# Optimization experiments

Hardware: AMD Instinct MI355X
Metric: run time of the kernel (lower is better)

## Reference

```python
import math
import jax, jax.numpy as jnp
import numpy as np

NUM_HEADS = 16
NEG = -1e30  # block-causal 'invisible' value (stand-in for -inf)
SCALES = [(1, 1, 1), (1, 2, 2), (1, 4, 4), (1, 8, 8), (1, 16, 16), (1, 32, 32)]


def _block_causal_bias(L):
    blocks = np.array([t * h * w for (t, h, w) in SCALES])
    cum = np.cumsum(blocks)  # visible kv length for each scale block
    per_query_visible = np.repeat(cum, blocks)  # (L,)
    cols = np.arange(L)
    mask = np.where(cols[None, :] < per_query_visible[:, None], 0.0, NEG).astype(np.float32)
    return jnp.asarray(mask)[None, None]  # (1,1,L,L)


def _rope_tables(L, half_dim):
    # 2D-rope-style cos/sin tables; exact frequency layout is data, math is the rotation
    pos = np.arange(L, dtype=np.float32)
    inv_freq = 1.0 / (10000.0 ** (np.arange(half_dim, dtype=np.float32) / half_dim))
    ang = pos[:, None] * inv_freq[None, :]  # (L, half_dim)
    return jnp.asarray(np.cos(ang)), jnp.asarray(np.sin(ang))


def setup_inputs() -> dict:
    key = jax.random.key(0)
    ks = jax.random.split(key, 6)
    B, C, H = 4, 1024, NUM_HEADS
    hd = C // H
    L = int(sum(t * h * w for (t, h, w) in SCALES))  # 1365
    x = jax.random.normal(ks[0], (B, L, C), dtype=jnp.float32)
    attn_bias = _block_causal_bias(L)
    rope_cos, rope_sin = _rope_tables(L, hd // 2)
    W_qkv = jax.random.normal(ks[1], (3 * C, C), dtype=jnp.float32) * (C ** -0.5)
    q_bias = jnp.zeros((C,), dtype=jnp.float32)
    v_bias = jnp.zeros((C,), dtype=jnp.float32)
    scale_mul_log = jnp.full((1, H, 1, 1), math.log(4.0), dtype=jnp.float32)
    W_proj = jax.random.normal(ks[2], (C, C), dtype=jnp.float32) * (C ** -0.5)
    b_proj = jnp.zeros((C,), dtype=jnp.float32)
    return {"x": x, "attn_bias": attn_bias, "rope_cos": rope_cos, "rope_sin": rope_sin,
            "W_qkv": W_qkv, "q_bias": q_bias, "v_bias": v_bias,
            "scale_mul_log": scale_mul_log, "W_proj": W_proj, "b_proj": b_proj}


def _apply_rope(t, rope_cos, rope_sin):
    # t: (B,H,L,hd) -> rotate consecutive pairs with per-position cos/sin
    B, H, L, hd = t.shape
    t2 = t.reshape(B, H, L, hd // 2, 2)
    c = rope_cos[None, None]  # (1,1,L,hd/2)
    s = rope_sin[None, None]
    r0 = c * t2[..., 0] - s * t2[..., 1]
    r1 = s * t2[..., 0] + c * t2[..., 1]
    return jnp.stack([r0, r1], axis=-1).reshape(B, H, L, hd)


def reference(x, attn_bias, rope_cos, rope_sin, W_qkv, q_bias, v_bias,
              scale_mul_log, W_proj, b_proj):
    B, L, C = x.shape
    H = NUM_HEADS
    hd = C // H
    # QKV with custom bias construction: (q_bias, zeros, v_bias)
    bias = jnp.concatenate([q_bias, jnp.zeros_like(q_bias), v_bias])
    qkv = (x @ W_qkv.T + bias).reshape(B, L, 3, H, hd)
    qkv = jnp.transpose(qkv, (2, 0, 3, 1, 4))  # (3,B,H,L,hd)
    q, k, v = qkv[0], qkv[1], qkv[2]
    # cos-attn: L2-normalize q,k; q scaled by clamped learnable per-head temperature
    max_scale_mul = math.log(100.0)
    scale_mul = jnp.exp(jnp.minimum(scale_mul_log, max_scale_mul))  # (1,H,1,1)
    q = q / jnp.maximum(jnp.linalg.norm(q, axis=-1, keepdims=True), 1e-12) * scale_mul
    k = k / jnp.maximum(jnp.linalg.norm(k, axis=-1, keepdims=True), 1e-12)
    # inline RoPE on q and k
    q = _apply_rope(q, rope_cos, rope_sin)
    k = _apply_rope(k, rope_cos, rope_sin)
    # block-causal attention; softmax scale = 1 under cos_attn
    logits = jnp.einsum('bhqd,bhkd->bhqk', q, k) + attn_bias
    attn = jax.nn.softmax(logits, axis=-1)
    out = jnp.einsum('bhqk,bhkd->bhqd', attn, v)
    out = jnp.transpose(out, (0, 2, 1, 3)).reshape(B, L, C)
    return out @ W_proj.T + b_proj
```

## Files before the change

### kernel.cpp

```cpp
#include <hip/hip_runtime.h>

typedef __bf16 bf16_t;
typedef __bf16 bf16x8 __attribute__((ext_vector_type(8)));
typedef float f32x4 __attribute__((ext_vector_type(4)));

#define B_SZ 4
#define NHEADS 16
#define L_SEQ 1365
#define LP_V 1408
#define C_DIM 1024
#define HD 64
#define M_ROWS (B_SZ * L_SEQ)
#define K_DIM 1024
#define BHL (B_SZ * NHEADS * L_SEQ)

__device__ __forceinline__ f32x4 zero4() {
    f32x4 z; z[0] = 0.f; z[1] = 0.f; z[2] = 0.f; z[3] = 0.f; return z;
}

__device__ __forceinline__ void gload_lds16(const void* g, void* l) {
    __builtin_amdgcn_global_load_lds(
        (const __attribute__((address_space(1))) void*)(uintptr_t)g,
        (__attribute__((address_space(3))) void*)(unsigned int)(uintptr_t)l,
        16, 0, 0);
}

__device__ __forceinline__ int vislen(int row) {
    if (row < 1) return 1;
    if (row < 5) return 5;
    if (row < 21) return 21;
    if (row < 85) return 85;
    if (row < 341) return 341;
    return 1365;
}

#define N8_X  (5591040 / 8)
#define N8_WQ (3145728 / 8)
#define N8_WP (1048576 / 8)
__global__ __launch_bounds__(256) void cvt_all(const float* __restrict__ x,
                                               const float* __restrict__ wq,
                                               const float* __restrict__ wp,
                                               bf16_t* __restrict__ xo,
                                               bf16_t* __restrict__ wqo,
                                               bf16_t* __restrict__ wpo) {
    int i = blockIdx.x * 256 + threadIdx.x;
    const float* in;
    bf16_t* out;
    if (i < N8_X) { in = x; out = xo; }
    else if (i < N8_X + N8_WQ) { i -= N8_X; in = wq; out = wqo; }
    else if (i < N8_X + N8_WQ + N8_WP) { i -= N8_X + N8_WQ; in = wp; out = wpo; }
    else return;
    const float* p = in + (size_t)i * 8;
    f32x4 a = *(const f32x4*)p;
    f32x4 b = *(const f32x4*)(p + 4);
    bf16x8 r;
    r[0] = (bf16_t)a[0]; r[1] = (bf16_t)a[1]; r[2] = (bf16_t)a[2]; r[3] = (bf16_t)a[3];
    r[4] = (bf16_t)b[0]; r[5] = (bf16_t)b[1]; r[6] = (bf16_t)b[2]; r[7] = (bf16_t)b[3];
    *(bf16x8*)(out + (size_t)i * 8) = r;
}

__global__ __launch_bounds__(256) void qkv_gemm(const bf16_t* __restrict__ A,
                                                const bf16_t* __restrict__ Bw,
                                                const float* __restrict__ qbias,
                                                const float* __restrict__ vbias,
                                                bf16_t* __restrict__ qo,
                                                bf16_t* __restrict__ ko,
                                                bf16_t* __restrict__ vt) {
    __shared__ __align__(16) bf16_t As[128 * 32];
    __shared__ __align__(16) bf16_t Bs[128 * 32];
    const int tid = threadIdx.x;
    const int w = tid >> 6, lane = tid & 63, quad = lane >> 4, l16 = lane & 15;
    const int id = blockIdx.x;
    const int xcd = id & 7, s = id >> 3;
    const int ntile = xcd * 3 + s / 43;
    const int mtile = s - (s / 43) * 43;
    const int mw = (w >> 1) * 64, nw = (w & 1) * 64;

    int ar0 = mtile * 128 + (tid >> 2); if (ar0 > M_ROWS - 1) ar0 = M_ROWS - 1;
    int ar1 = ar0 + 64;                 if (ar1 > M_ROWS - 1) ar1 = M_ROWS - 1;
    const int nr0 = ntile * 128 + (tid >> 2);
    const int cc = (tid & 3) * 8;

    f32x4 acc[4][4];
#pragma unroll
    for (int i = 0; i < 4; ++i)
#pragma unroll
        for (int j = 0; j < 4; ++j) acc[i][j] = zero4();

    for (int k0 = 0; k0 < K_DIM; k0 += 32) {
        __syncthreads();
        gload_lds16(A + (size_t)ar0 * K_DIM + k0 + cc, (char*)As + tid * 16);
        gload_lds16(A + (size_t)ar1 * K_DIM + k0 + cc, (char*)As + tid * 16 + 4096);
        gload_lds16(Bw + (size_t)nr0 * K_DIM + k0 + cc, (char*)Bs + tid * 16);
        gload_lds16(Bw + (size_t)(nr0 + 64) * K_DIM + k0 + cc, (char*)Bs + tid * 16 + 4096);
        __syncthreads();
        bf16x8 af[4], bfr[4];
#pragma unroll
        for (int mi = 0; mi < 4; ++mi)
            af[mi] = *(const bf16x8*)&As[(mw + mi * 16 + l16) * 32 + quad * 8];
#pragma unroll
        for (int ni = 0; ni < 4; ++ni)
            bfr[ni] = *(const bf16x8*)&Bs[(nw + ni * 16 + l16) * 32 + quad * 8];
#pragma unroll
        for (int mi = 0; mi < 4; ++mi)
#pragma unroll
            for (int ni = 0; ni < 4; ++ni)
                acc[mi][ni] = __builtin_amdgcn_mfma_f32_16x16x32_bf16(af[mi], bfr[ni], acc[mi][ni], 0, 0, 0);
    }

#pragma unroll
    for (int ni = 0; ni < 4; ++ni) {
        int ncol = ntile * 128 + nw + ni * 16 + l16;
        int three = ncol >> 10;
        int rem = ncol & 1023;
        int h = rem >> 6, d = rem & 63;
        float bias = 0.f;
        if (three == 0) bias = qbias[rem];
        else if (three == 2) bias = vbias[rem];
        bf16_t* dst = (three == 0) ? qo : ((three == 1) ? ko : vt);
#pragma unroll
        for (int mi = 0; mi < 4; ++mi)
#pragma unroll
            for (int r = 0; r < 4; ++r) {
                int grow = mtile * 128 + mw + mi * 16 + quad * 4 + r;
                if (grow < M_ROWS) {
                    int b_ = grow / L_SEQ;
                    int l = grow - b_ * L_SEQ;
                    dst[(((size_t)(b_ * NHEADS + h)) * L_SEQ + l) * HD + d] =
                        (bf16_t)(acc[mi][ni][r] + bias);
                }
            }
    }
}

__global__ __launch_bounds__(256) void vtrans(const bf16_t* __restrict__ in,
                                              bf16_t* __restrict__ out) {
    __shared__ bf16_t t[64][64];
    const int lt = blockIdx.x * 64, bh = blockIdx.y;
    const int tid = threadIdx.x;
#pragma unroll
    for (int it = 0; it < 2; ++it) {
        const int r = (tid >> 3) + it * 32, c8 = (tid & 7) * 8;
        int l = lt + r; if (l > L_SEQ - 1) l = L_SEQ - 1;
        bf16x8 v8 = *(const bf16x8*)(in + ((size_t)bh * L_SEQ + l) * HD + c8);
#pragma unroll
        for (int j = 0; j < 8; ++j) t[c8 + j][r] = v8[j];
    }
    __syncthreads();
#pragma unroll
    for (int it = 0; it < 2; ++it) {
        int c = tid + it * 256;
        int d = c >> 3, off = (c & 7) * 8;
        bf16x8 o8 = *(const bf16x8*)&t[d][off];
        *(bf16x8*)(out + ((size_t)bh * HD + d) * LP_V + lt + off) = o8;
    }
}

__global__ __launch_bounds__(256) void normrope(bf16_t* __restrict__ qb,
                                                bf16_t* __restrict__ kb,
                                                const float* __restrict__ cosb,
                                                const float* __restrict__ sinb,
                                                const float* __restrict__ sml) {
    const int tid = threadIdx.x;
    const int w = tid >> 6, lane = tid & 63;
    int vi = blockIdx.x * 4 + w;
    bool isq = vi < BHL;
    int idx = isq ? vi : (vi - BHL);
    bf16_t* buf = isq ? qb : kb;
    int bh = idx / L_SEQ;
    int l = idx - bh * L_SEQ;
    int h = bh & (NHEADS - 1);
    size_t base = (size_t)idx * HD;

    float v = (float)buf[base + lane];
    float ss = v * v;
#pragma unroll
    for (int off = 1; off < 64; off <<= 1) ss += __shfl_xor(ss, off);
    float nrm = fmaxf(sqrtf(ss), 1e-12f);
    v = v / nrm;
    if (isq) {
        float s = expf(fminf(sml[h], 4.6051702f));
        v *= s;
    }
    int i = lane >> 1;
    float c = cosb[l * 32 + i];
    float s2 = sinb[l * 32 + i];
    float p = __shfl_xor(v, 1);
    float r = (lane & 1) ? (s2 * p + c * v) : (c * v - s2 * p);
    buf[base + lane] = (bf16_t)r;
}

__global__ __launch_bounds__(256) void attn(const bf16_t* __restrict__ q,
                                            const bf16_t* __restrict__ k,
                                            const bf16_t* __restrict__ v,
                                            bf16_t* __restrict__ ao) {
    __shared__ __align__(16) bf16_t plds[4][2][16][72];
    const int tid = threadIdx.x;
    const int w = tid >> 6, lane = tid & 63, quad = lane >> 4, l16 = lane & 15;
    const int id = blockIdx.x;
    const int xcd = id & 7, s0 = id >> 3;
    const int bh = (xcd << 3) + s0 / 11;
    const int gblk = s0 - (s0 / 11) * 11;
    const int g = gblk + 11 * w;
    if (g >= 43) return;
    const int qbase = g * 32;

    bf16x8 aq[2][2];
#pragma unroll
    for (int h = 0; h < 2; ++h) {
        int mrow = qbase + h * 16 + l16;
        int mc = mrow < L_SEQ ? mrow : (L_SEQ - 1);
        const bf16_t* qp = q + ((size_t)bh * L_SEQ + mc) * HD + quad * 8;
        aq[h][0] = *(const bf16x8*)(qp);
        aq[h][1] = *(const bf16x8*)(qp + 32);
    }

    f32x4 o[2][4];
    float l_i[2][4];
    int visr[2][4];
#pragma unroll
    for (int h = 0; h < 2; ++h)
#pragma unroll
        for (int r = 0; r < 4; ++r) {
            o[h][r] = zero4();
            l_i[h][r] = 0.f;
            visr[h][r] = vislen(qbase + h * 16 + quad * 4 + r);
        }

    int rl = qbase + 31; if (rl > L_SEQ - 1) rl = L_SEQ - 1;
    const int ntk = (vislen(rl) + 63) >> 6;

    for (int kt = 0; kt < ntk; ++kt) {
        const int kvb = kt * 64;
        bf16x8 kf0[4], kf1[4];
#pragma unroll
        for (int nb = 0; nb < 4; ++nb) {
            int n = kvb + nb * 16 + l16;
            int nc = n < L_SEQ ? n : (L_SEQ - 1);
            const bf16_t* kp = k + ((size_t)bh * L_SEQ + nc) * HD + quad * 8;
            kf0[nb] = *(const bf16x8*)(kp);
            kf1[nb] = *(const bf16x8*)(kp + 32);
        }
        f32x4 s[2][4];
#pragma unroll
        for (int h = 0; h < 2; ++h)
#pragma unroll
            for (int nb = 0; nb < 4; ++nb) {
                s[h][nb] = zero4();
                s[h][nb] = __builtin_amdgcn_mfma_f32_16x16x32_bf16(aq[h][0], kf0[nb], s[h][nb], 0, 0, 0);
                s[h][nb] = __builtin_amdgcn_mfma_f32_16x16x32_bf16(aq[h][1], kf1[nb], s[h][nb], 0, 0, 0);
            }

#pragma unroll
        for (int h = 0; h < 2; ++h)
#pragma unroll
            for (int nb = 0; nb < 4; ++nb) {
                int col = kvb + nb * 16 + l16;
#pragma unroll
                for (int r = 0; r < 4; ++r) {
                    float e = __expf(s[h][nb][r]);
                    float p = (col < visr[h][r]) ? e : 0.f;
                    l_i[h][r] += p;
                    plds[w][h][quad * 4 + r][nb * 16 + l16] = (bf16_t)p;
                }
            }
        bf16x8 ap[2][2];
#pragma unroll
        for (int h = 0; h < 2; ++h) {
            ap[h][0] = *(const bf16x8*)&plds[w][h][l16][quad * 8];
            ap[h][1] = *(const bf16x8*)&plds[w][h][l16][32 + quad * 8];
        }
#pragma unroll
        for (int nb = 0; nb < 4; ++nb) {
            const bf16_t* vp = v + ((size_t)bh * HD + nb * 16 + l16) * LP_V + kvb + quad * 8;
            bf16x8 v0 = *(const bf16x8*)(vp);
            bf16x8 v1 = *(const bf16x8*)(vp + 32);
#pragma unroll
            for (int h = 0; h < 2; ++h) {
                o[h][nb] = __builtin_amdgcn_mfma_f32_16x16x32_bf16(ap[h][0], v0, o[h][nb], 0, 0, 0);
                o[h][nb] = __builtin_amdgcn_mfma_f32_16x16x32_bf16(ap[h][1], v1, o[h][nb], 0, 0, 0);
            }
        }
    }

    const int b_ = bh >> 4, hh = bh & 15;
#pragma unroll
    for (int h = 0; h < 2; ++h)
#pragma unroll
        for (int r = 0; r < 4; ++r) {
            float ls = l_i[h][r];
#pragma unroll
            for (int off = 1; off < 16; off <<= 1) ls += __shfl_xor(ls, off);
            int rowq = qbase + h * 16 + quad * 4 + r;
            if (rowq < L_SEQ) {
                float inv = 1.f / ls;
#pragma unroll
                for (int nb = 0; nb < 4; ++nb) {
                    int d = nb * 16 + l16;
                    size_t di = ((size_t)(b_ * L_SEQ + rowq)) * C_DIM + hh * HD + d;
                    ao[di] = (bf16_t)(o[h][nb][r] * inv);
                }
            }
        }
}

__global__ __launch_bounds__(256) void proj_gemm(const bf16_t* __restrict__ A,
                                                 const bf16_t* __restrict__ Bw,
                                                 const float* __restrict__ bias,
                                                 float* __restrict__ out) {
    __shared__ __align__(16) bf16_t As[128 * 32];
    __shared__ __align__(16) bf16_t Bs[128 * 32];
    const int tid = threadIdx.x;
    const int w = tid >> 6, lane = tid & 63, quad = lane >> 4, l16 = lane & 15;
    const int id = blockIdx.x;
    const int ntile = id & 7, mtile = id >> 3;
    const int mw = (w >> 1) * 64, nw = (w & 1) * 64;

    int ar0 = mtile * 128 + (tid >> 2); if (ar0 > M_ROWS - 1) ar0 = M_ROWS - 1;
    int ar1 = ar0 + 64;                 if (ar1 > M_ROWS - 1) ar1 = M_ROWS - 1;
    const int nr0 = ntile * 128 + (tid >> 2);
    const int cc = (tid & 3) * 8;

    f32x4 acc[4][4];
#pragma unroll
    for (int i = 0; i < 4; ++i)
#pragma unroll
        for (int j = 0; j < 4; ++j) acc[i][j] = zero4();

    for (int k0 = 0; k0 < K_DIM; k0 += 32) {
        __syncthreads();
        gload_lds16(A + (size_t)ar0 * K_DIM + k0 + cc, (char*)As + tid * 16);
        gload_lds16(A + (size_t)ar1 * K_DIM + k0 + cc, (char*)As + tid * 16 + 4096);
        gload_lds16(Bw + (size_t)nr0 * K_DIM + k0 + cc, (char*)Bs + tid * 16);
        gload_lds16(Bw + (size_t)(nr0 + 64) * K_DIM + k0 + cc, (char*)Bs + tid * 16 + 4096);
        __syncthreads();
        bf16x8 af[4], bfr[4];
#pragma unroll
        for (int mi = 0; mi < 4; ++mi)
            af[mi] = *(const bf16x8*)&As[(mw + mi * 16 + l16) * 32 + quad * 8];
#pragma unroll
        for (int ni = 0; ni < 4; ++ni)
            bfr[ni] = *(const bf16x8*)&Bs[(nw + ni * 16 + l16) * 32 + quad * 8];
#pragma unroll
        for (int mi = 0; mi < 4; ++mi)
#pragma unroll
            for (int ni = 0; ni < 4; ++ni)
                acc[mi][ni] = __builtin_amdgcn_mfma_f32_16x16x32_bf16(af[mi], bfr[ni], acc[mi][ni], 0, 0, 0);
    }

#pragma unroll
    for (int ni = 0; ni < 4; ++ni) {
        int ncol = ntile * 128 + nw + ni * 16 + l16;
        float bv = bias[ncol];
#pragma unroll
        for (int mi = 0; mi < 4; ++mi)
#pragma unroll
            for (int r = 0; r < 4; ++r) {
                int grow = mtile * 128 + mw + mi * 16 + quad * 4 + r;
                if (grow < M_ROWS)
                    out[(size_t)grow * C_DIM + ncol] = acc[mi][ni][r] + bv;
            }
    }
}

extern "C" void kernel_launch(void* const* d_in, const int* in_sizes, int n_in,
                              void* d_out, int out_size, void* d_ws, size_t ws_size,
                              hipStream_t stream) {
    const float* x    = (const float*)d_in[0];
    const float* rc   = (const float*)d_in[2];
    const float* rs   = (const float*)d_in[3];
    const float* Wqkv = (const float*)d_in[4];
    const float* qb   = (const float*)d_in[5];
    const float* vb   = (const float*)d_in[6];
    const float* sml  = (const float*)d_in[7];
    const float* Wp   = (const float*)d_in[8];
    const float* bp   = (const float*)d_in[9];
    float* out = (float*)d_out;

    const size_t NQ   = (size_t)B_SZ * NHEADS * L_SEQ * HD;
    const size_t NVT  = (size_t)B_SZ * NHEADS * HD * LP_V;
    const size_t NX   = (size_t)M_ROWS * C_DIM;
    const size_t NWQ  = (size_t)3 * C_DIM * C_DIM;
    const size_t NWP  = (size_t)C_DIM * C_DIM;

    bf16_t* qo   = (bf16_t*)d_ws;
    bf16_t* ko   = qo + NQ;
    bf16_t* vtmp = ko + NQ;
    bf16_t* vo   = vtmp + NQ;
    bf16_t* xb   = vo + NVT;
    bf16_t* ao   = xb;
    bf16_t* wqb  = xb + NX;
    bf16_t* wpb  = wqb + NWQ;

    dim3 blk(256);
    const int ncvt = (N8_X + N8_WQ + N8_WP + 255) / 256;
    cvt_all<<<dim3(ncvt), blk, 0, stream>>>(x, Wqkv, Wp, xb, wqb, wpb);
    qkv_gemm<<<dim3(1032), blk, 0, stream>>>(xb, wqb, qb, vb, qo, ko, vtmp);
    normrope<<<dim3((2 * BHL) / 4), blk, 0, stream>>>(qo, ko, rc, rs, sml);
    vtrans<<<dim3(22, 64), blk, 0, stream>>>(vtmp, vo);
    attn<<<dim3(704), blk, 0, stream>>>(qo, ko, vo, ao);
    proj_gemm<<<dim3(344), blk, 0, stream>>>(ao, wpb, bp, out);
}
```

Baseline: 335.9 us.

## Fuse norm+RoPE into QKV epilogue and split-KV the last attention scale

Removes the separate normrope kernel by applying L2 norm, per-head temperature and RoPE in the QKV GEMM epilogue using cross-lane shuffles. Attention work is rebalanced: the long last-scale query groups (vislen 1365) are split into two KV chunks written as fp32 partials and combined by a new attn_reduce kernel, while short groups write output directly. This targets load imbalance in attention and the extra q/k round trip through memory, at the cost of partial-buffer traffic and an extra launch. Split partials are summed without max rescaling, which relies on the bounded cos-attn logits.

```diff
diff --git a/kernel.cpp b/kernel.cpp
--- a/kernel.cpp
+++ b/kernel.cpp
@@ -13,6 +13,11 @@
 #define M_ROWS (B_SZ * L_SEQ)
 #define K_DIM 1024
 #define BHL (B_SZ * NHEADS * L_SEQ)
+
+#define NSPLIT 33
+#define NCHUNK 2
+#define UPB (10 + NSPLIT * NCHUNK)
+#define NBLK_ATTN (64 * UPB / 4)
 
 __device__ __forceinline__ f32x4 zero4() {
     f32x4 z; z[0] = 0.f; z[1] = 0.f; z[2] = 0.f; z[3] = 0.f; return z;
@@ -63,6 +68,9 @@
                                                 const bf16_t* __restrict__ Bw,
                                                 const float* __restrict__ qbias,
                                                 const float* __restrict__ vbias,
+                                                const float* __restrict__ rc,
+                                                const float* __restrict__ rs,
+                                                const float* __restrict__ sml,
                                                 bf16_t* __restrict__ qo,
                                                 bf16_t* __restrict__ ko,
                                                 bf16_t* __restrict__ vt) {
@@ -108,26 +116,63 @@
                 acc[mi][ni] = __builtin_amdgcn_mfma_f32_16x16x32_bf16(af[mi], bfr[ni], acc[mi][ni], 0, 0, 0);
     }
 
-#pragma unroll
-    for (int ni = 0; ni < 4; ++ni) {
-        int ncol = ntile * 128 + nw + ni * 16 + l16;
-        int three = ncol >> 10;
-        int rem = ncol & 1023;
-        int h = rem >> 6, d = rem & 63;
-        float bias = 0.f;
-        if (three == 0) bias = qbias[rem];
-        else if (three == 2) bias = vbias[rem];
-        bf16_t* dst = (three == 0) ? qo : ((three == 1) ? ko : vt);
+    const int three = ntile >> 3;
+    const int h = (((ntile & 7) * 128 + nw) >> 6);
+
+    if (three == 2) {
+#pragma unroll
+        for (int ni = 0; ni < 4; ++ni) {
+            int d = ni * 16 + l16;
+            float bv = vbias[h * 64 + d];
+#pragma unroll
+            for (int mi = 0; mi < 4; ++mi)
+#pragma unroll
+                for (int r = 0; r < 4; ++r) {
+                    int grow = mtile * 128 + mw + mi * 16 + quad * 4 + r;
+                    if (grow < M_ROWS) {
+                        int b_ = grow / L_SEQ;
+                        int l = grow - b_ * L_SEQ;
+                        vt[(((size_t)(b_ * NHEADS + h)) * L_SEQ + l) * HD + d] =
+                            (bf16_t)(acc[mi][ni][r] + bv);
+                    }
+                }
+        }
+    } else {
+        float scale = 1.f;
+        if (three == 0) scale = __expf(fminf(sml[h], 4.6051702f));
+        float bias[4];
+#pragma unroll
+        for (int ni = 0; ni < 4; ++ni)
+            bias[ni] = (three == 0) ? qbias[h * 64 + ni * 16 + l16] : 0.f;
+        bf16_t* dst = (three == 0) ? qo : ko;
 #pragma unroll
         for (int mi = 0; mi < 4; ++mi)
 #pragma unroll
             for (int r = 0; r < 4; ++r) {
                 int grow = mtile * 128 + mw + mi * 16 + quad * 4 + r;
-                if (grow < M_ROWS) {
-                    int b_ = grow / L_SEQ;
-                    int l = grow - b_ * L_SEQ;
-                    dst[(((size_t)(b_ * NHEADS + h)) * L_SEQ + l) * HD + d] =
-                        (bf16_t)(acc[mi][ni][r] + bias);
+                float vv[4];
+                float ss = 0.f;
+#pragma unroll
+                for (int ni = 0; ni < 4; ++ni) {
+                    vv[ni] = acc[mi][ni][r] + bias[ni];
+                    ss += vv[ni] * vv[ni];
+                }
+                ss += __shfl_xor(ss, 1); ss += __shfl_xor(ss, 2);
+                ss += __shfl_xor(ss, 4); ss += __shfl_xor(ss, 8);
+                float inv = scale * rsqrtf(fmaxf(ss, 1e-24f));
+                int gc = grow < M_ROWS ? grow : M_ROWS - 1;
+                int b_ = gc / L_SEQ;
+                int l = gc - b_ * L_SEQ;
+#pragma unroll
+                for (int ni = 0; ni < 4; ++ni) {
+                    float vn = vv[ni] * inv;
+                    float pp = __shfl_xor(vn, 1);
+                    int ti = l * 32 + ni * 8 + (l16 >> 1);
+                    float c = rc[ti], s2 = rs[ti];
+                    float ov = (l16 & 1) ? (s2 * pp + c * vn) : (c * vn - s2 * pp);
+                    if (grow < M_ROWS)
+                        dst[(((size_t)(b_ * NHEADS + h)) * L_SEQ + l) * HD + ni * 16 + l16] =
+                            (bf16_t)ov;
                 }
             }
     }
@@ -156,53 +201,32 @@
     }
 }
 
-__global__ __launch_bounds__(256) void normrope(bf16_t* __restrict__ qb,
-                                                bf16_t* __restrict__ kb,
-                                                const float* __restrict__ cosb,
-                                                const float* __restrict__ sinb,
-                                                const float* __restrict__ sml) {
-    const int tid = threadIdx.x;
-    const int w = tid >> 6, lane = tid & 63;
-    int vi = blockIdx.x * 4 + w;
-    bool isq = vi < BHL;
-    int idx = isq ? vi : (vi - BHL);
-    bf16_t* buf = isq ? qb : kb;
-    int bh = idx / L_SEQ;
-    int l = idx - bh * L_SEQ;
-    int h = bh & (NHEADS - 1);
-    size_t base = (size_t)idx * HD;
-
-    float v = (float)buf[base + lane];
-    float ss = v * v;
-#pragma unroll
-    for (int off = 1; off < 64; off <<= 1) ss += __shfl_xor(ss, off);
-    float nrm = fmaxf(sqrtf(ss), 1e-12f);
-    v = v / nrm;
-    if (isq) {
-        float s = expf(fminf(sml[h], 4.6051702f));
-        v *= s;
-    }
-    int i = lane >> 1;
-    float c = cosb[l * 32 + i];
-    float s2 = sinb[l * 32 + i];
-    float p = __shfl_xor(v, 1);
-    float r = (lane & 1) ? (s2 * p + c * v) : (c * v - s2 * p);
-    buf[base + lane] = (bf16_t)r;
-}
-
 __global__ __launch_bounds__(256) void attn(const bf16_t* __restrict__ q,
                                             const bf16_t* __restrict__ k,
                                             const bf16_t* __restrict__ v,
-                                            bf16_t* __restrict__ ao) {
+                                            bf16_t* __restrict__ ao,
+                                            float* __restrict__ OP,
+                                            float* __restrict__ LPb) {
     __shared__ __align__(16) bf16_t plds[4][2][16][72];
     const int tid = threadIdx.x;
     const int w = tid >> 6, lane = tid & 63, quad = lane >> 4, l16 = lane & 15;
-    const int id = blockIdx.x;
-    const int xcd = id & 7, s0 = id >> 3;
-    const int bh = (xcd << 3) + s0 / 11;
-    const int gblk = s0 - (s0 / 11) * 11;
-    const int g = gblk + 11 * w;
-    if (g >= 43) return;
+    const int bid = blockIdx.x;
+    const int xcd = bid & 7, s0 = bid >> 3;
+    const int bh = (xcd << 3) + s0 / 19;
+    const int ublk = s0 - (s0 / 19) * 19;
+    const int u = ublk * 4 + w;
+    int g, t0, t1, ck = 0;
+    bool direct;
+    if (u < 10) { g = u; t0 = 0; t1 = (u < 2) ? 2 : 6; direct = true; }
+    else {
+        int t = u - 10;
+        int gi = t >> 1;
+        ck = t & 1;
+        g = 10 + gi;
+        t0 = ck * 11;
+        t1 = t0 + 11;
+        direct = false;
+    }
     const int qbase = g * 32;
 
     bf16x8 aq[2][2];
@@ -227,10 +251,7 @@
             visr[h][r] = vislen(qbase + h * 16 + quad * 4 + r);
         }
 
-    int rl = qbase + 31; if (rl > L_SEQ - 1) rl = L_SEQ - 1;
-    const int ntk = (vislen(rl) + 63) >> 6;
-
-    for (int kt = 0; kt < ntk; ++kt) {
+    for (int kt = t0; kt < t1; ++kt) {
         const int kvb = kt * 64;
         bf16x8 kf0[4], kf1[4];
 #pragma unroll
@@ -283,25 +304,86 @@
         }
     }
 
+    if (direct) {
+        const int b_ = bh >> 4, hh = bh & 15;
+#pragma unroll
+        for (int h = 0; h < 2; ++h)
+#pragma unroll
+            for (int r = 0; r < 4; ++r) {
+                float ls = l_i[h][r];
+#pragma unroll
+                for (int off = 1; off < 16; off <<= 1) ls += __shfl_xor(ls, off);
+                int rowq = qbase + h * 16 + quad * 4 + r;
+                if (rowq < L_SEQ) {
+                    float inv = 1.f / ls;
+#pragma unroll
+                    for (int nb = 0; nb < 4; ++nb) {
+                        int d = nb * 16 + l16;
+                        size_t di = ((size_t)(b_ * L_SEQ + rowq)) * C_DIM + hh * HD + d;
+                        ao[di] = (bf16_t)(o[h][nb][r] * inv);
+                    }
+                }
+            }
+    } else {
+        const int g9 = g - 10;
+        size_t ub = (((size_t)ck * 64 + bh) * NSPLIT + g9) * 2048;
+#pragma unroll
+        for (int h = 0; h < 2; ++h)
+#pragma unroll
+            for (int nb = 0; nb < 4; ++nb)
+                *(f32x4*)(OP + ub + (size_t)((h * 4 + nb) * 64 + lane) * 4) = o[h][nb];
+        size_t lb = (((size_t)ck * 64 + bh) * NSPLIT + g9) * 32;
+#pragma unroll
+        for (int h = 0; h < 2; ++h)
+#pragma unroll
+            for (int r = 0; r < 4; ++r) {
+                float ls = l_i[h][r];
+#pragma unroll
+                for (int off = 1; off < 16; off <<= 1) ls += __shfl_xor(ls, off);
+                if (l16 == 0) LPb[lb + h * 16 + quad * 4 + r] = ls;
+            }
+    }
+}
+
+__global__ __launch_bounds__(256) void attn_reduce(const float* __restrict__ OP,
+                                                   const float* __restrict__ LPb,
+                                                   bf16_t* __restrict__ ao) {
+    __shared__ float lsum[32];
+    const int bid = blockIdx.x;
+    const int xcd = bid & 7, s = bid >> 3;
+    const int bh = (xcd << 3) + s / 33;
+    const int g9 = s - (s / 33) * 33;
+    const int tid = threadIdx.x;
+    if (tid < 32) {
+        float sm = 0.f;
+#pragma unroll
+        for (int ck = 0; ck < NCHUNK; ++ck)
+            sm += LPb[(((size_t)ck * 64 + bh) * NSPLIT + g9) * 32 + tid];
+        lsum[tid] = sm;
+    }
+    __syncthreads();
+    const int lane = tid & 63, p = tid >> 6;
+    const int quad = lane >> 4, l16 = lane & 15;
+    const int qbase = (g9 + 10) * 32;
     const int b_ = bh >> 4, hh = bh & 15;
-#pragma unroll
-    for (int h = 0; h < 2; ++h)
+    size_t ub = ((size_t)bh * NSPLIT + g9) * 2048;
+#pragma unroll
+    for (int h = 0; h < 2; ++h) {
+        f32x4 acc = zero4();
+#pragma unroll
+        for (int ck = 0; ck < NCHUNK; ++ck)
+            acc += *(const f32x4*)(OP + (size_t)ck * 64 * NSPLIT * 2048 + ub +
+                                   (size_t)((h * 4 + p) * 64 + lane) * 4);
+        int col = p * 16 + l16;
 #pragma unroll
         for (int r = 0; r < 4; ++r) {
-            float ls = l_i[h][r];
-#pragma unroll
-            for (int off = 1; off < 16; off <<= 1) ls += __shfl_xor(ls, off);
-            int rowq = qbase + h * 16 + quad * 4 + r;
-            if (rowq < L_SEQ) {
-                float inv = 1.f / ls;
-#pragma unroll
-                for (int nb = 0; nb < 4; ++nb) {
-                    int d = nb * 16 + l16;
-                    size_t di = ((size_t)(b_ * L_SEQ + rowq)) * C_DIM + hh * HD + d;
-                    ao[di] = (bf16_t)(o[h][nb][r] * inv);
-                }
-            }
-        }
+            int row = h * 16 + quad * 4 + r;
+            int rowq = qbase + row;
+            if (rowq < L_SEQ)
+                ao[((size_t)(b_ * L_SEQ + rowq)) * C_DIM + hh * HD + col] =
+                    (bf16_t)(acc[r] / lsum[row]);
+        }
+    }
 }
 
 __global__ __launch_bounds__(256) void proj_gemm(const bf16_t* __restrict__ A,
@@ -391,13 +473,15 @@
     bf16_t* ao   = xb;
     bf16_t* wqb  = xb + NX;
     bf16_t* wpb  = wqb + NWQ;
+    float*  OPb  = (float*)(wpb + NWP);
+    float*  LPb  = OPb + (size_t)NCHUNK * 64 * NSPLIT * 2048;
 
     dim3 blk(256);
     const int ncvt = (N8_X + N8_WQ + N8_WP + 255) / 256;
     cvt_all<<<dim3(ncvt), blk, 0, stream>>>(x, Wqkv, Wp, xb, wqb, wpb);
-    qkv_gemm<<<dim3(1032), blk, 0, stream>>>(xb, wqb, qb, vb, qo, ko, vtmp);
-    normrope<<<dim3((2 * BHL) / 4), blk, 0, stream>>>(qo, ko, rc, rs, sml);
+    qkv_gemm<<<dim3(1032), blk, 0, stream>>>(xb, wqb, qb, vb, rc, rs, sml, qo, ko, vtmp);
     vtrans<<<dim3(22, 64), blk, 0, stream>>>(vtmp, vo);
-    attn<<<dim3(704), blk, 0, stream>>>(qo, ko, vo, ao);
+    attn<<<dim3(NBLK_ATTN), blk, 0, stream>>>(qo, ko, vo, ao, OPb, LPb);
+    attn_reduce<<<dim3(2112), blk, 0, stream>>>(OPb, LPb, ao);
     proj_gemm<<<dim3(344), blk, 0, stream>>>(ao, wpb, bp, out);
 }
```

Result: slower. 346.3 us (+3.1%).
